# Kernel tuning notes

Hardware: AMD Instinct MI355X
Metric: run time of the kernel (lower is better)

The kernel has to match this reference:

```python
import jax, jax.numpy as jnp
import numpy as np
from jax import lax

N_ENT = 20000; N_REL = 256; H = 512; C = 64; K = 3; L = 2; T = 8; E = 30000; B = 4096


def _seg_mean(vals, ids, num_segments):
    s = jax.ops.segment_sum(vals, ids, num_segments=num_segments)
    c = jax.ops.segment_sum(jnp.ones(ids.shape, vals.dtype), ids, num_segments=num_segments)
    return s / jnp.maximum(c, 1.0)[:, None]


def _normalize(x, eps=1e-8):
    return x / (jnp.linalg.norm(x, axis=-1, keepdims=True) + eps)


def _gru(x, h, Wih, Whh, bih, bhh):
    gi = x @ Wih + bih
    gh = h @ Whh + bhh
    ir, iz, inn = jnp.split(gi, 3, axis=-1)
    hr, hz, hn = jnp.split(gh, 3, axis=-1)
    r = jax.nn.sigmoid(ir + hr)
    z = jax.nn.sigmoid(iz + hz)
    n = jnp.tanh(inn + r * hn)
    return (1.0 - z) * n + z * h


def _backbone(x, convW, convB, fcW, fcB):
    # x: (B, Cin, H) -> (B, H); ConvTrans backbone: 1D 'same' conv over hidden dim,
    # relu, flatten, linear projection back to H, relu (BN identity at init, dropout=eval)
    h = lax.conv_general_dilated(x, convW, (1,), 'SAME', dimension_numbers=('NCH', 'OIH', 'NCH'))
    h = jax.nn.relu(h + convB[None, :, None])
    h = h.reshape(h.shape[0], -1)
    return jax.nn.relu(h @ fcW + fcB)


def _forward(ent_embeds, rel_embeds, W_msg, W_self, gru_Wih, gru_Whh, gru_bih, gru_bhh,
             gate_W, gate_b,
             e_conv1, e_cb1, e_fc1, e_fb1, e_conv2, e_cb2, e_fc2, e_fb2,
             r_conv1, r_cb1, r_fc1, r_fb1, r_conv2, r_cb2, r_fc2, r_fb2,
             src, dst, erel, subj, rel, obj):
    def step(carry, xs):
        ent, relh = carry
        s, d, r = xs
        # relation evolution: aggregate incident-entity embeds per relation, GRU with static rel embeds
        agg = _seg_mean(ent[s], r, N_REL)                                   # (R, H)
        relh = _gru(jnp.concatenate([agg, rel_embeds], -1), relh, gru_Wih, gru_Whh, gru_bih, gru_bhh)
        # entity evolution: L layers of RGCN-style message passing over the snapshot
        h = ent
        for l in range(L):
            msg = (h[s] + relh[r]) @ W_msg[l]                               # (E, H)
            h = jax.nn.relu(_seg_mean(msg, d, N_ENT) + h @ W_self[l])
        h = _normalize(h)
        u = jax.nn.sigmoid(h @ gate_W + gate_b)                             # time gate
        ent = u * h + (1.0 - u) * ent
        return (ent, relh), None

    (ent, relh), _ = lax.scan(step, (_normalize(ent_embeds), rel_embeds), (src, dst, erel))

    se = ent[subj]
    re_ = relh[rel]
    oe = ent[obj]
    # RefineConvTransE (object prediction)
    o1 = _backbone(jnp.stack([se, re_], 1), e_conv1, e_cb1, e_fc1, e_fb1)
    o2 = _backbone(jnp.stack([o1, se, re_], 1), e_conv2, e_cb2, e_fc2, e_fb2)
    # RefineConvTransR (relation prediction)
    q1 = _backbone(jnp.stack([se, oe], 1), r_conv1, r_cb1, r_fc1, r_fb1)
    q2 = _backbone(jnp.stack([q1, se, oe], 1), r_conv2, r_cb2, r_fc2, r_fb2)
    return (o1 @ ent.T, q1 @ relh.T, o2 @ ent.T, q2 @ relh.T)


def setup_inputs() -> dict:
    key = jax.random.key(0)
    ks = jax.random.split(key, 32)
    f = lambda i, shape, s=0.02: jax.random.normal(ks[i], shape, jnp.float32) * s
    return dict(
        ent_embeds=f(0, (N_ENT, H), 0.05),
        rel_embeds=f(1, (N_REL, H), 0.05),
        W_msg=f(2, (L, H, H)),
        W_self=f(3, (L, H, H)),
        gru_Wih=f(4, (2 * H, 3 * H)),
        gru_Whh=f(5, (H, 3 * H)),
        gru_bih=jnp.zeros((3 * H,), jnp.float32),
        gru_bhh=jnp.zeros((3 * H,), jnp.float32),
        gate_W=f(6, (H, H)),
        gate_b=jnp.zeros((H,), jnp.float32),
        e_conv1=f(7, (C, 2, K)), e_cb1=jnp.zeros((C,), jnp.float32),
        e_fc1=f(8, (C * H, H)), e_fb1=jnp.zeros((H,), jnp.float32),
        e_conv2=f(9, (C, 3, K)), e_cb2=jnp.zeros((C,), jnp.float32),
        e_fc2=f(10, (C * H, H)), e_fb2=jnp.zeros((H,), jnp.float32),
        r_conv1=f(11, (C, 2, K)), r_cb1=jnp.zeros((C,), jnp.float32),
        r_fc1=f(12, (C * H, H)), r_fb1=jnp.zeros((H,), jnp.float32),
        r_conv2=f(13, (C, 3, K)), r_cb2=jnp.zeros((C,), jnp.float32),
        r_fc2=f(14, (C * H, H)), r_fb2=jnp.zeros((H,), jnp.float32),
        src=jax.random.randint(ks[15], (T, E), 0, N_ENT),
        dst=jax.random.randint(ks[16], (T, E), 0, N_ENT),
        erel=jax.random.randint(ks[17], (T, E), 0, N_REL),
        subj=jax.random.randint(ks[18], (B,), 0, N_ENT),
        rel=jax.random.randint(ks[19], (B,), 0, N_REL),
        obj=jax.random.randint(ks[20], (B,), 0, N_ENT),
    )


def reference(ent_embeds, rel_embeds, W_msg, W_self, gru_Wih, gru_Whh, gru_bih, gru_bhh,
              gate_W, gate_b,
              e_conv1, e_cb1, e_fc1, e_fb1, e_conv2, e_cb2, e_fc2, e_fb2,
              r_conv1, r_cb1, r_fc1, r_fb1, r_conv2, r_cb2, r_fc2, r_fb2,
              src, dst, erel, subj, rel, obj):
    # returns (obj_logit_ori, rel_logit_ori, obj_logit, rel_logit)
    return _forward(ent_embeds, rel_embeds, W_msg, W_self, gru_Wih, gru_Whh, gru_bih, gru_bhh,
                    gate_W, gate_b,
                    e_conv1, e_cb1, e_fc1, e_fb1, e_conv2, e_cb2, e_fc2, e_fb2,
                    r_conv1, r_cb1, r_fc1, r_fb1, r_conv2, r_cb2, r_fc2, r_fb2,
                    src, dst, erel, subj, rel, obj)
```

## Files before the change

### kernel.cpp

```cpp
#include <hip/hip_runtime.h>
#include <math.h>


#define N_ENT 20000
#define N_REL 256
#define HD    512
#define NE    30000
#define NB    4096
#define NT    8

typedef __attribute__((ext_vector_type(8))) short          bf16x8;
typedef __attribute__((ext_vector_type(4))) float          f32x4;
typedef __attribute__((ext_vector_type(8))) unsigned short u16x8;
typedef __attribute__((ext_vector_type(4))) unsigned short u16x4;

static __device__ __forceinline__ float sigmoidf_(float x) {
  return 1.0f / (1.0f + expf(-x));
}
static __device__ __forceinline__ unsigned short f2bf(float f) {
  unsigned u = __float_as_uint(f);
  return (unsigned short)((u + 0x7FFFu + ((u >> 16) & 1u)) >> 16);
}

__global__ void rownorm_kernel(const float* __restrict__ in, float* __restrict__ out,
                               unsigned short* __restrict__ outb, int rows) {
  int wid = (blockIdx.x * blockDim.x + threadIdx.x) >> 6;
  int lane = threadIdx.x & 63;
  if (wid >= rows) return;
  const float4* ip = (const float4*)(in + (size_t)wid * HD);
  float4 v0 = ip[lane];
  float4 v1 = ip[lane + 64];
  float s = v0.x * v0.x + v0.y * v0.y + v0.z * v0.z + v0.w * v0.w
          + v1.x * v1.x + v1.y * v1.y + v1.z * v1.z + v1.w * v1.w;
  #pragma unroll
  for (int m = 1; m < 64; m <<= 1) s += __shfl_xor(s, m);
  float inv = 1.0f / (sqrtf(s) + 1e-8f);
  float4* op = (float4*)(out + (size_t)wid * HD);
  v0.x *= inv; v0.y *= inv; v0.z *= inv; v0.w *= inv;
  v1.x *= inv; v1.y *= inv; v1.z *= inv; v1.w *= inv;
  op[lane] = v0; op[lane + 64] = v1;
  unsigned short* ob = outb + (size_t)wid * HD;
  u16x4 p0 = {f2bf(v0.x), f2bf(v0.y), f2bf(v0.z), f2bf(v0.w)};
  u16x4 p1 = {f2bf(v1.x), f2bf(v1.y), f2bf(v1.z), f2bf(v1.w)};
  *(u16x4*)&ob[lane * 4] = p0;
  *(u16x4*)&ob[(lane + 64) * 4] = p1;
}

__global__ void zero_hist_all(int* __restrict__ h) {
  int i = blockIdx.x * 256 + threadIdx.x;
  if (i < NT * (N_ENT + N_REL)) h[i] = 0;
}

__global__ void hist_all(const int* __restrict__ dst, const int* __restrict__ rel,
                         int* __restrict__ histD8, int* __restrict__ histR8) {
  int e = blockIdx.x * 256 + threadIdx.x;
  int t = blockIdx.y;
  if (e >= NE) return;
  atomicAdd(&histD8[t * N_ENT + dst[t * NE + e]], 1);
  atomicAdd(&histR8[t * N_REL + rel[t * NE + e]], 1);
}

__global__ void scan_part_all(const int* __restrict__ histD8, int* __restrict__ partD8) {
  int t = blockIdx.x, tid = threadIdx.x;
  const int* hd = histD8 + t * N_ENT;
  int base = tid * 80;
  int s = 0;
  for (int i = 0; i < 80; ++i) {
    int idx = base + i;
    if (idx < N_ENT) s += hd[idx];
  }
  partD8[t * 257 + tid] = s;
}

__global__ void scan_serial_all(int* __restrict__ partD8, const int* __restrict__ histR8,
                                int* __restrict__ startR8, int* __restrict__ posR8) {
  int t = blockIdx.x;
  int* pd = partD8 + t * 257;
  int run = 0;
  for (int i = 0; i < 256; ++i) { int v = pd[i]; pd[i] = run; run += v; }
  pd[256] = run;
  const int* hr = histR8 + t * N_REL;
  int* sr = startR8 + t * 257;
  int* pr = posR8 + t * N_REL;
  run = 0;
  for (int i = 0; i < 256; ++i) { int v = hr[i]; sr[i] = run; pr[i] = run; run += v; }
  sr[256] = run;
}

__global__ void scan_local_all(const int* __restrict__ histD8, const int* __restrict__ partD8,
                               int* __restrict__ startD8, int* __restrict__ posD8) {
  int t = blockIdx.x, tid = threadIdx.x;
  const int* hd = histD8 + t * N_ENT;
  int* sd = startD8 + t * (N_ENT + 1);
  int* pd = posD8 + t * N_ENT;
  int run = partD8[t * 257 + tid];
  int base = tid * 80;
  for (int i = 0; i < 80; ++i) {
    int idx = base + i;
    if (idx < N_ENT) {
      sd[idx] = run;
      pd[idx] = run;
      run += hd[idx];
    }
  }
  if (tid == 0) sd[N_ENT] = partD8[t * 257 + 256];
}

__global__ void scatter_all(const int* __restrict__ dst, const int* __restrict__ rel,
                            int* __restrict__ posD8, int* __restrict__ posR8,
                            int* __restrict__ edgeD8, int* __restrict__ edgeR8) {
  int e = blockIdx.x * 256 + threadIdx.x;
  int t = blockIdx.y;
  if (e >= NE) return;
  int p = atomicAdd(&posD8[t * N_ENT + dst[t * NE + e]], 1);
  edgeD8[t * NE + p] = e;
  int p2 = atomicAdd(&posR8[t * N_REL + rel[t * NE + e]], 1);
  edgeR8[t * NE + p2] = e;
}

__global__ __launch_bounds__(256)
void agg_rel_csr(const float* __restrict__ ent, const int* __restrict__ src,
                 const int* __restrict__ edgeR, const int* __restrict__ startR,
                 float* __restrict__ aggR, float* __restrict__ cntR) {
  int r = blockIdx.x * 4 + (threadIdx.x >> 6);
  if (r >= N_REL) return;
  int lane = threadIdx.x & 63;
  int s0 = startR[r], s1 = startR[r + 1];
  float4 a = make_float4(0.f, 0.f, 0.f, 0.f);
  float4 b = make_float4(0.f, 0.f, 0.f, 0.f);
  for (int i = s0; i < s1; ++i) {
    int e = edgeR[i];
    int s = src[e];
    const float4* p = (const float4*)(ent + (size_t)s * HD);
    float4 x = p[lane];
    float4 y = p[lane + 64];
    a.x += x.x; a.y += x.y; a.z += x.z; a.w += x.w;
    b.x += y.x; b.y += y.y; b.z += y.z; b.w += y.w;
  }
  float4* op = (float4*)(aggR + (size_t)r * HD);
  op[lane] = a;
  op[lane + 64] = b;
  if (lane == 0) cntR[r] = (float)(s1 - s0);
}

__global__ __launch_bounds__(256)
void agg_ent_csr(const float* __restrict__ h, const float* __restrict__ relh,
                 const int* __restrict__ src, const int* __restrict__ erel,
                 const int* __restrict__ edgeD, const int* __restrict__ startD,
                 float* __restrict__ aggE, float* __restrict__ cntE) {
  int d = blockIdx.x * 4 + (threadIdx.x >> 6);
  if (d >= N_ENT) return;
  int lane = threadIdx.x & 63;
  int s0 = startD[d], s1 = startD[d + 1];
  float4 a = make_float4(0.f, 0.f, 0.f, 0.f);
  float4 b = make_float4(0.f, 0.f, 0.f, 0.f);
  for (int i = s0; i < s1; ++i) {
    int e = edgeD[i];
    int s = src[e], r = erel[e];
    const float4* hp = (const float4*)(h + (size_t)s * HD);
    const float4* rp = (const float4*)(relh + (size_t)r * HD);
    float4 x = hp[lane];
    float4 y = hp[lane + 64];
    float4 u = rp[lane];
    float4 v = rp[lane + 64];
    a.x += x.x + u.x; a.y += x.y + u.y; a.z += x.z + u.z; a.w += x.w + u.w;
    b.x += y.x + v.x; b.y += y.y + v.y; b.z += y.z + v.z; b.w += y.w + v.w;
  }
  float4* op = (float4*)(aggE + (size_t)d * HD);
  op[lane] = a;
  op[lane + 64] = b;
  if (lane == 0) cntE[d] = (float)(s1 - s0);
}

__global__ void gru_kernel(const float* __restrict__ gi, const float* __restrict__ gh,
                           const float* __restrict__ bih, const float* __restrict__ bhh,
                           float* __restrict__ relh, unsigned short* __restrict__ relhb) {
  int i = blockIdx.x * blockDim.x + threadIdx.x;
  if (i >= N_REL * HD) return;
  int row = i >> 9, col = i & 511;
  const float* gir = gi + (size_t)row * 1536;
  const float* ghr = gh + (size_t)row * 1536;
  float ir = gir[col] + bih[col];
  float iz = gir[col + 512] + bih[col + 512];
  float inn = gir[col + 1024] + bih[col + 1024];
  float hr = ghr[col] + bhh[col];
  float hz = ghr[col + 512] + bhh[col + 512];
  float hn = ghr[col + 1024] + bhh[col + 1024];
  float r = sigmoidf_(ir + hr);
  float z = sigmoidf_(iz + hz);
  float n = tanhf(inn + r * hn);
  float v = (1.0f - z) * n + z * relh[i];
  relh[i] = v;
  relhb[i] = f2bf(v);
}

__global__ void gather_kernel(const float* __restrict__ table, const int* __restrict__ idx,
                              float* __restrict__ out, int rows) {
  int i = blockIdx.x * blockDim.x + threadIdx.x;
  if (i >= rows * (HD / 4)) return;
  int row = i >> 7, q = i & 127;
  ((float4*)out)[i] = ((const float4*)(table + (size_t)idx[row] * HD))[q];
}

__global__ void f2b_kernel(const float* __restrict__ in, unsigned short* __restrict__ out, int n) {
  int i = blockIdx.x * blockDim.x + threadIdx.x;
  if (i * 8 >= n) return;
  float4 a = *(const float4*)&in[i * 8];
  float4 b = *(const float4*)&in[i * 8 + 4];
  u16x8 pk = {f2bf(a.x), f2bf(a.y), f2bf(a.z), f2bf(a.w),
              f2bf(b.x), f2bf(b.y), f2bf(b.z), f2bf(b.w)};
  *(u16x8*)&out[i * 8] = pk;
}

__global__ void pack_nn_kernel(const float* __restrict__ B, unsigned short* __restrict__ out,
                               int K, int N) {
  int id = blockIdx.x * 256 + threadIdx.x;
  if (id >= (K >> 3) * N) return;
  int s = id / (N * 4);
  int rem = id - s * (N * 4);
  int n = rem >> 2, g = rem & 3;
  const float* src = B + (size_t)(s * 32 + g * 8) * N + n;
  u16x8 pk;
  #pragma unroll
  for (int j = 0; j < 8; ++j) pk[j] = f2bf(src[(size_t)j * N]);
  *(u16x8*)&out[((size_t)s * N + n) * 32 + ((g ^ ((n >> 2) & 3)) << 3)] = pk;
}

template <int ACT, int MIRROR>
static __device__ __forceinline__
void gemm_core(const float* __restrict__ A0, int K0, const float* __restrict__ cntA,
               const unsigned short* __restrict__ A1, int K1,
               const unsigned short* __restrict__ Bp,
               const float* __restrict__ bias, const float* __restrict__ D,
               float* __restrict__ C, unsigned short* __restrict__ Cb,
               int M, int N, int m0, int n0,
               unsigned short (*As)[4096], unsigned short (*Bs)[4096]) {
  const int tid = threadIdx.x;
  const int lane = tid & 63;
  const int wv = tid >> 6;
  const int wm = wv >> 1, wn = wv & 1;
  const int lr = lane & 15, lg = lane >> 4;
  const int arow = tid >> 1;
  const int ahalf = tid & 1;
  const int NIT = (K0 + K1) >> 5;

  float s0 = 1.0f;
  if (K0 > 0 && (m0 + arow) < M) s0 = 1.0f / fmaxf(cntA[m0 + arow], 1.0f);

  f32x4 acc[4][4];
  #pragma unroll
  for (int i = 0; i < 4; ++i)
    #pragma unroll
    for (int j = 0; j < 4; ++j) acc[i][j] = (f32x4){0.f, 0.f, 0.f, 0.f};

  auto gload = [&](int it, u16x8* ar, u16x8* br) {
    int mrow = m0 + arow;
    int kk = it * 32 + ahalf * 16;
    if (mrow < M) {
      if (kk < K0) {
        const float* p = A0 + (size_t)mrow * K0 + kk;
        #pragma unroll
        for (int q = 0; q < 2; ++q) {
          float4 x = *(const float4*)(p + q * 8);
          float4 y = *(const float4*)(p + q * 8 + 4);
          ar[q] = (u16x8){f2bf(x.x * s0), f2bf(x.y * s0), f2bf(x.z * s0), f2bf(x.w * s0),
                          f2bf(y.x * s0), f2bf(y.y * s0), f2bf(y.z * s0), f2bf(y.w * s0)};
        }
      } else {
        const unsigned short* p = A1 + (size_t)mrow * K1 + (kk - K0);
        #pragma unroll
        for (int q = 0; q < 2; ++q) ar[q] = *(const u16x8*)&p[q * 8];
      }
    } else {
      #pragma unroll
      for (int q = 0; q < 2; ++q) ar[q] = (u16x8){0, 0, 0, 0, 0, 0, 0, 0};
    }
    const unsigned short* b0 = Bp + ((size_t)it * N + n0) * 32;
    br[0] = *(const u16x8*)&b0[tid * 8];
    br[1] = *(const u16x8*)&b0[2048 + tid * 8];
  };
  auto swrite = [&](int nb, const u16x8* ar, const u16x8* br) {
    #pragma unroll
    for (int q = 0; q < 2; ++q) {
      int chunk = ahalf * 2 + q;
      *(u16x8*)&As[nb][arow * 32 + ((chunk ^ ((arow >> 1) & 3)) << 3)] = ar[q];
    }
    *(u16x8*)&Bs[nb][tid * 8] = br[0];
    *(u16x8*)&Bs[nb][2048 + tid * 8] = br[1];
  };
  auto mfma_phase = [&](int nb) {
    bf16x8 a[4], b[4];
    #pragma unroll
    for (int i = 0; i < 4; ++i) {
      int r = wm * 64 + i * 16 + lr;
      a[i] = *(const bf16x8*)&As[nb][r * 32 + ((lg ^ ((r >> 1) & 3)) << 3)];
      int nl = wn * 64 + i * 16 + lr;
      b[i] = *(const bf16x8*)&Bs[nb][nl * 32 + ((lg ^ ((nl >> 2) & 3)) << 3)];
    }
    #pragma unroll
    for (int i = 0; i < 4; ++i)
      #pragma unroll
      for (int j = 0; j < 4; ++j)
        acc[i][j] = __builtin_amdgcn_mfma_f32_16x16x32_bf16(a[i], b[j], acc[i][j], 0, 0, 0);
  };

  u16x8 ar0[2], br0[2], ar1[2], br1[2];
  gload(0, ar0, br0);
  swrite(0, ar0, br0);
  gload(1, ar1, br1);
  __syncthreads();

  int cur = 0;
  for (int itp = 0; itp < NIT; itp += 2) {
    if (itp + 2 < NIT) gload(itp + 2, ar0, br0);
    mfma_phase(cur);
    swrite(cur ^ 1, ar1, br1);
    __syncthreads();
    cur ^= 1;
    if (itp + 3 < NIT) gload(itp + 3, ar1, br1);
    mfma_phase(cur);
    if (itp + 2 < NIT) swrite(cur ^ 1, ar0, br0);
    __syncthreads();
    cur ^= 1;
  }

  #pragma unroll
  for (int i = 0; i < 4; ++i) {
    int m = m0 + wm * 64 + i * 16 + lg * 4;
    #pragma unroll
    for (int j = 0; j < 4; ++j) {
      int n = n0 + wn * 64 + j * 16 + lr;
      #pragma unroll
      for (int q = 0; q < 4; ++q) {
        int mr = m + q;
        if (mr >= M) continue;
        size_t o = (size_t)mr * N + n;
        float v = acc[i][j][q];
        if (ACT == 0) {
          C[o] = v;
        } else if (ACT == 1) {
          float rr = fmaxf(v, 0.0f);
          C[o] = rr;
          if (MIRROR) Cb[o] = f2bf(rr);
        } else {
          float u_ = sigmoidf_(v + bias[n]);
          float rr = u_ * D[o] + (1.0f - u_) * C[o];
          C[o] = rr;
          if (MIRROR) Cb[o] = f2bf(rr);
        }
      }
    }
  }
}

template <int ACT, int MIRROR>
__global__ __launch_bounds__(256, 3)
void gemm_nn2(const float* __restrict__ A0, int K0, const float* __restrict__ cntA,
              const unsigned short* __restrict__ A1, int K1,
              const unsigned short* __restrict__ Bp,
              const float* __restrict__ bias, const float* __restrict__ D,
              float* __restrict__ C, unsigned short* __restrict__ Cb, int M, int N) {
  __shared__ unsigned short As[2][4096];
  __shared__ unsigned short Bs[2][4096];
  gemm_core<ACT, MIRROR>(A0, K0, cntA, A1, K1, Bp, bias, D, C, Cb, M, N,
                         blockIdx.x * 128, blockIdx.y * 128, As, Bs);
}

__global__ __launch_bounds__(256, 3)
void gru_gemms(const float* __restrict__ aggR, const float* __restrict__ cntR,
               const unsigned short* __restrict__ rel_bf,
               const unsigned short* __restrict__ relh_bf,
               const unsigned short* __restrict__ wp_ih,
               const unsigned short* __restrict__ wp_hh,
               float* __restrict__ gi, float* __restrict__ gh) {
  __shared__ unsigned short As[2][4096];
  __shared__ unsigned short Bs[2][4096];
  if (blockIdx.z == 0)
    gemm_core<0, 0>(aggR, 512, cntR, rel_bf, 512, wp_ih, nullptr, nullptr,
                    gi, nullptr, N_REL, 1536, blockIdx.x * 128, blockIdx.y * 128, As, Bs);
  else
    gemm_core<0, 0>(nullptr, 0, nullptr, relh_bf, 512, wp_hh, nullptr, nullptr,
                    gh, nullptr, N_REL, 1536, blockIdx.x * 128, blockIdx.y * 128, As, Bs);
}

__global__ __launch_bounds__(256)
void pack_fw_kernel(const float* __restrict__ f0, const float* __restrict__ f1,
                    const float* __restrict__ f2, const float* __restrict__ f3,
                    unsigned short* __restrict__ o0, unsigned short* __restrict__ o1,
                    unsigned short* __restrict__ o2, unsigned short* __restrict__ o3) {
  __shared__ float L[32][512];
  const float* fw; unsigned short* op;
  switch (blockIdx.y) {
    case 0: fw = f0; op = o0; break;
    case 1: fw = f1; op = o1; break;
    case 2: fw = f2; op = o2; break;
    default: fw = f3; op = o3; break;
  }
  int s = blockIdx.x, tid = threadIdx.x;
  #pragma unroll
  for (int i = 0; i < 16; ++i) {
    int idx = tid + 256 * i;
    int r = idx >> 7, cq = (idx & 127) << 2;
    *(float4*)&L[r][cq] = *(const float4*)&fw[(size_t)(s * 32 + r) * 512 + cq];
  }
  __syncthreads();
  #pragma unroll
  for (int ii = 0; ii < 8; ++ii) {
    int slot = tid + 256 * ii;
    int n = slot >> 2, g = slot & 3;
    u16x8 pk;
    #pragma unroll
    for (int j = 0; j < 8; ++j) pk[j] = f2bf(L[g * 8 + j][n]);
    size_t off = (size_t)s * 16384 + n * 32 + ((g ^ ((n >> 2) & 3)) << 3);
    *(u16x8*)&op[off] = pk;
  }
}

template <int CIN>
__global__ __launch_bounds__(256)
void convgen_kernel(const float* __restrict__ X0e, const float* __restrict__ X1e,
                    const float* __restrict__ X2e,
                    const float* __restrict__ cwE, const float* __restrict__ cbE,
                    const float* __restrict__ X0r, const float* __restrict__ X1r,
                    const float* __restrict__ X2r,
                    const float* __restrict__ cwR, const float* __restrict__ cbR,
                    unsigned short* __restrict__ Ae, unsigned short* __restrict__ Ar) {
  __shared__ float wsm[64 * CIN * 3];
  __shared__ float bsm[64];
  const int path = blockIdx.y;
  const float* X[CIN]; const float* cw; const float* cb; unsigned short* A;
  if (path == 0) {
    X[0] = X0e; X[1] = X1e; if constexpr (CIN == 3) X[2] = X2e;
    cw = cwE; cb = cbE; A = Ae;
  } else {
    X[0] = X0r; X[1] = X1r; if constexpr (CIN == 3) X[2] = X2r;
    cw = cwR; cb = cbR; A = Ar;
  }
  const int tid = threadIdx.x;
  for (int i = tid; i < 64 * CIN * 3; i += 256) wsm[i] = cw[i];
  if (tid < 64) bsm[tid] = cb[tid];
  __syncthreads();

  const int o = tid & 63;
  const int b = blockIdx.x * 4 + (tid >> 6);
  const int h = o * 8;

  float xm[CIN][8], xl[CIN], xr[CIN];
  #pragma unroll
  for (int ci = 0; ci < CIN; ++ci) {
    const float* row = X[ci] + (size_t)b * HD + h;
    float4 a4 = *(const float4*)row;
    float4 b4 = *(const float4*)(row + 4);
    xm[ci][0] = a4.x; xm[ci][1] = a4.y; xm[ci][2] = a4.z; xm[ci][3] = a4.w;
    xm[ci][4] = b4.x; xm[ci][5] = b4.y; xm[ci][6] = b4.z; xm[ci][7] = b4.w;
    xl[ci] = (h > 0) ? row[-1] : 0.f;
    xr[ci] = (h + 8 < HD) ? row[8] : 0.f;
  }
  unsigned short* dst = A + (size_t)b * 32768 + h;
  for (int c = 0; c < 64; ++c) {
    float v[8];
    float cbv = bsm[c];
    #pragma unroll
    for (int e = 0; e < 8; ++e) v[e] = cbv;
    #pragma unroll
    for (int ci = 0; ci < CIN; ++ci) {
      float w0 = wsm[(c * CIN + ci) * 3 + 0];
      float w1 = wsm[(c * CIN + ci) * 3 + 1];
      float w2 = wsm[(c * CIN + ci) * 3 + 2];
      #pragma unroll
      for (int e = 0; e < 8; ++e) {
        float lft = e ? xm[ci][e - 1] : xl[ci];
        float rgt = (e < 7) ? xm[ci][e + 1] : xr[ci];
        v[e] = fmaf(lft, w0, fmaf(xm[ci][e], w1, fmaf(rgt, w2, v[e])));
      }
    }
    u16x8 pk;
    #pragma unroll
    for (int e = 0; e < 8; ++e) pk[e] = f2bf(fmaxf(v[e], 0.f));
    *(u16x8*)&dst[c * 512] = pk;
  }
}

__global__ __launch_bounds__(256, 2)
void gemm_fc(const unsigned short* __restrict__ Abuf,
             const unsigned short* __restrict__ fwpE,
             const unsigned short* __restrict__ fwpR,
             float* __restrict__ partBase) {
  __shared__ unsigned short As[2][128 * 64];
  __shared__ unsigned short Bs[2][2 * 128 * 32];
  const int tid = threadIdx.x;
  const int lane = tid & 63;
  const int wv = tid >> 6;
  const int wm = wv >> 1, wn = wv & 1;
  const int lr = lane & 15, lg = lane >> 4;
  const int m0 = blockIdx.x * 128;
  const int n0 = blockIdx.y * 128;
  const int path = blockIdx.z >> 2;
  const int ks = blockIdx.z & 3;

  const unsigned short* A = Abuf + (size_t)path * ((size_t)NB * 32768);
  const unsigned short* fwp = (path == 0) ? fwpE : fwpR;
  float* part = partBase + (size_t)(path * 4 + ks) * ((size_t)NB * HD);

  const int arow = tid >> 1;
  const int achunk = (tid & 1) * 4;
  const unsigned short* aRow = A + (size_t)(m0 + arow) * 32768 + ks * 8192 + achunk * 8;
  const unsigned short* bBase = fwp + (size_t)(ks * 256) * 16384 + (size_t)n0 * 32;

  f32x4 acc[4][4];
  #pragma unroll
  for (int i = 0; i < 4; ++i)
    #pragma unroll
    for (int j = 0; j < 4; ++j) acc[i][j] = (f32x4){0.f, 0.f, 0.f, 0.f};

  auto gload = [&](int it, u16x8* ar, u16x8* br) {
    const unsigned short* ap = aRow + it * 64;
    #pragma unroll
    for (int q = 0; q < 4; ++q) ar[q] = *(const u16x8*)&ap[q * 8];
    const unsigned short* bp = bBase + (size_t)it * 2 * 16384;
    br[0] = *(const u16x8*)&bp[tid * 8];
    br[1] = *(const u16x8*)&bp[2048 + tid * 8];
    br[2] = *(const u16x8*)&bp[16384 + tid * 8];
    br[3] = *(const u16x8*)&bp[16384 + 2048 + tid * 8];
  };
  auto swrite = [&](int nb, const u16x8* ar, const u16x8* br) {
    #pragma unroll
    for (int q = 0; q < 4; ++q) {
      int chunk = achunk + q;
      *(u16x8*)&As[nb][arow * 64 + ((chunk ^ (arow & 7)) << 3)] = ar[q];
    }
    *(u16x8*)&Bs[nb][tid * 8] = br[0];
    *(u16x8*)&Bs[nb][2048 + tid * 8] = br[1];
    *(u16x8*)&Bs[nb][4096 + tid * 8] = br[2];
    *(u16x8*)&Bs[nb][4096 + 2048 + tid * 8] = br[3];
  };
  auto mfma_phase = [&](int nb) {
    bf16x8 af[2][4], bfr[2][4];
    #pragma unroll
    for (int u = 0; u < 2; ++u)
      #pragma unroll
      for (int i = 0; i < 4; ++i) {
        int r = wm * 64 + i * 16 + lr;
        af[u][i] = *(const bf16x8*)&As[nb][r * 64 + (((u * 4 + lg) ^ (r & 7)) << 3)];
        int nl = wn * 64 + i * 16 + lr;
        bfr[u][i] = *(const bf16x8*)&Bs[nb][u * 4096 + nl * 32 + ((lg ^ ((nl >> 2) & 3)) << 3)];
      }
    #pragma unroll
    for (int u = 0; u < 2; ++u)
      #pragma unroll
      for (int i = 0; i < 4; ++i)
        #pragma unroll
        for (int j = 0; j < 4; ++j)
          acc[i][j] = __builtin_amdgcn_mfma_f32_16x16x32_bf16(af[u][i], bfr[u][j], acc[i][j], 0, 0, 0);
  };

  u16x8 ar0[4], br0[4], ar1[4], br1[4];
  gload(0, ar0, br0);
  swrite(0, ar0, br0);
  gload(1, ar1, br1);
  __syncthreads();

  int cur = 0;
  for (int itp = 0; itp < 128; itp += 2) {
    if (itp + 2 < 128) gload(itp + 2, ar0, br0);
    mfma_phase(cur);
    swrite(cur ^ 1, ar1, br1);
    __syncthreads();
    cur ^= 1;
    if (itp + 3 < 128) gload(itp + 3, ar1, br1);
    mfma_phase(cur);
    if (itp + 2 < 128) swrite(cur ^ 1, ar0, br0);
    __syncthreads();
    cur ^= 1;
  }

  #pragma unroll
  for (int i = 0; i < 4; ++i) {
    int m = m0 + wm * 64 + i * 16 + lg * 4;
    #pragma unroll
    for (int j = 0; j < 4; ++j) {
      int n = n0 + wn * 64 + j * 16 + lr;
      #pragma unroll
      for (int q = 0; q < 4; ++q)
        part[(size_t)(m + q) * HD + n] = acc[i][j][q];
    }
  }
}

__global__ void reduce4_kernel(const float* __restrict__ pE, const float* __restrict__ pR,
                               const float* __restrict__ bE, const float* __restrict__ bR,
                               float* __restrict__ oE, float* __restrict__ oR,
                               unsigned short* __restrict__ obE, unsigned short* __restrict__ obR) {
  int p = blockIdx.y;
  const float* part = p ? pR : pE;
  const float* bias = p ? bR : bE;
  float* o = p ? oR : oE;
  unsigned short* ob = p ? obR : obE;
  int i = blockIdx.x * 256 + threadIdx.x;
  int col = (i << 2) & 511;
  float4 s = *(const float4*)&part[(size_t)i * 4];
  #pragma unroll
  for (int ks = 1; ks < 4; ++ks) {
    float4 t = *(const float4*)&part[(size_t)ks * (NB * HD) + i * 4];
    s.x += t.x; s.y += t.y; s.z += t.z; s.w += t.w;
  }
  float4 b4 = *(const float4*)&bias[col];
  s.x = fmaxf(s.x + b4.x, 0.f); s.y = fmaxf(s.y + b4.y, 0.f);
  s.z = fmaxf(s.z + b4.z, 0.f); s.w = fmaxf(s.w + b4.w, 0.f);
  *(float4*)&o[(size_t)i * 4] = s;
  u16x4 pk = {f2bf(s.x), f2bf(s.y), f2bf(s.z), f2bf(s.w)};
  *(u16x4*)&ob[(size_t)i * 4] = pk;
}

__global__ __launch_bounds__(256, 2)
void gemm_nt_bf16(const unsigned short* __restrict__ A, const unsigned short* __restrict__ B,
                  float* __restrict__ C, int M, int N, int K) {
  __shared__ unsigned short As[2][8192];
  __shared__ unsigned short Bs[2][8192];
  const int tid = threadIdx.x;
  const int lane = tid & 63;
  const int wv = tid >> 6;
  const int wm = wv >> 1, wn = wv & 1;
  const int m0 = blockIdx.x * 128, n0 = blockIdx.y * 128;
  const int lr = lane & 15, lg = lane >> 4;
  const int row = tid >> 1, half = tid & 1;
  const int nrow = n0 + row;
  const int NIT = K >> 6;

  f32x4 acc[4][4];
  #pragma unroll
  for (int i = 0; i < 4; ++i)
    #pragma unroll
    for (int j = 0; j < 4; ++j) acc[i][j] = (f32x4){0.f, 0.f, 0.f, 0.f};

  auto gload = [&](int it, u16x8* ar, u16x8* br) {
    const unsigned short* asrc = A + (size_t)(m0 + row) * K + it * 64 + half * 32;
    #pragma unroll
    for (int q = 0; q < 4; ++q) ar[q] = *(const u16x8*)&asrc[q * 8];
    const unsigned short* bsrc = B + (size_t)nrow * K + it * 64 + half * 32;
    u16x8 z = {0, 0, 0, 0, 0, 0, 0, 0};
    #pragma unroll
    for (int q = 0; q < 4; ++q) br[q] = (nrow < N) ? *(const u16x8*)&bsrc[q * 8] : z;
  };
  auto swrite = [&](int nb, const u16x8* ar, const u16x8* br) {
    #pragma unroll
    for (int q = 0; q < 4; ++q) {
      int chunk = half * 4 + q;
      *(u16x8*)&As[nb][row * 64 + ((chunk ^ (row & 7)) << 3)] = ar[q];
      *(u16x8*)&Bs[nb][row * 64 + ((chunk ^ (row & 7)) << 3)] = br[q];
    }
  };
  auto mfma_phase = [&](int nb) {
    #pragma unroll
    for (int u = 0; u < 2; ++u) {
      bf16x8 a[4], b[4];
      #pragma unroll
      for (int i = 0; i < 4; ++i) {
        int r = wm * 64 + i * 16 + lr;
        a[i] = *(const bf16x8*)&As[nb][r * 64 + (((u * 4 + lg) ^ (r & 7)) << 3)];
        int n = wn * 64 + i * 16 + lr;
        b[i] = *(const bf16x8*)&Bs[nb][n * 64 + (((u * 4 + lg) ^ (n & 7)) << 3)];
      }
      #pragma unroll
      for (int i = 0; i < 4; ++i)
        #pragma unroll
        for (int j = 0; j < 4; ++j)
          acc[i][j] = __builtin_amdgcn_mfma_f32_16x16x32_bf16(a[i], b[j], acc[i][j], 0, 0, 0);
    }
  };

  u16x8 ar0[4], br0[4], ar1[4], br1[4];
  gload(0, ar0, br0);
  swrite(0, ar0, br0);
  gload(1, ar1, br1);
  __syncthreads();

  int cur = 0;
  for (int itp = 0; itp < NIT; itp += 2) {
    if (itp + 2 < NIT) gload(itp + 2, ar0, br0);
    mfma_phase(cur);
    swrite(cur ^ 1, ar1, br1);
    __syncthreads();
    cur ^= 1;
    if (itp + 3 < NIT) gload(itp + 3, ar1, br1);
    mfma_phase(cur);
    if (itp + 2 < NIT) swrite(cur ^ 1, ar0, br0);
    __syncthreads();
    cur ^= 1;
  }

  #pragma unroll
  for (int i = 0; i < 4; ++i) {
    int m = m0 + wm * 64 + i * 16 + lg * 4;
    #pragma unroll
    for (int j = 0; j < 4; ++j) {
      int n = n0 + wn * 64 + j * 16 + lr;
      if (n < N) {
        #pragma unroll
        for (int q = 0; q < 4; ++q)
          C[(size_t)(m + q) * N + n] = acc[i][j][q];
      }
    }
  }
}

extern "C" void kernel_launch(void* const* d_in, const int* in_sizes, int n_in,
                              void* d_out, int out_size, void* d_ws, size_t ws_size,
                              hipStream_t stream) {
  const float* ent_embeds = (const float*)d_in[0];
  const float* rel_embeds = (const float*)d_in[1];
  const float* W_msg  = (const float*)d_in[2];
  const float* W_self = (const float*)d_in[3];
  const float* gru_Wih = (const float*)d_in[4];
  const float* gru_Whh = (const float*)d_in[5];
  const float* gru_bih = (const float*)d_in[6];
  const float* gru_bhh = (const float*)d_in[7];
  const float* gate_W = (const float*)d_in[8];
  const float* gate_b = (const float*)d_in[9];
  const float* e_conv1 = (const float*)d_in[10]; const float* e_cb1 = (const float*)d_in[11];
  const float* e_fc1   = (const float*)d_in[12]; const float* e_fb1 = (const float*)d_in[13];
  const float* e_conv2 = (const float*)d_in[14]; const float* e_cb2 = (const float*)d_in[15];
  const float* e_fc2   = (const float*)d_in[16]; const float* e_fb2 = (const float*)d_in[17];
  const float* r_conv1 = (const float*)d_in[18]; const float* r_cb1 = (const float*)d_in[19];
  const float* r_fc1   = (const float*)d_in[20]; const float* r_fb1 = (const float*)d_in[21];
  const float* r_conv2 = (const float*)d_in[22]; const float* r_cb2 = (const float*)d_in[23];
  const float* r_fc2   = (const float*)d_in[24]; const float* r_fb2 = (const float*)d_in[25];
  const int* src  = (const int*)d_in[26];
  const int* dst  = (const int*)d_in[27];
  const int* erel = (const int*)d_in[28];
  const int* subj = (const int*)d_in[29];
  const int* rel  = (const int*)d_in[30];
  const int* obj  = (const int*)d_in[31];
  float* out = (float*)d_out;

  float* w = (float*)d_ws;
  float* ent   = w; w += (size_t)N_ENT * HD;
  float* relh  = w; w += (size_t)N_REL * HD;
  float* aggR  = w; w += (size_t)N_REL * HD;
  float* cntR  = w; w += N_REL;
  float* gi    = w; w += (size_t)N_REL * 1536;
  float* gh    = w; w += (size_t)N_REL * 1536;
  float* aggE  = w; w += (size_t)N_ENT * HD;
  float* cntE  = w; w += N_ENT;
  float* tmp   = w; w += (size_t)N_ENT * HD;
  float* h0b   = w; w += (size_t)N_ENT * HD;
  float* h1b   = w; w += (size_t)N_ENT * HD;
  float* se    = w; w += (size_t)NB * HD;
  float* re_   = w; w += (size_t)NB * HD;
  float* oe    = w; w += (size_t)NB * HD;
  float* o1    = w; w += (size_t)NB * HD;
  float* q1    = w; w += (size_t)NB * HD;
  float* o2    = w; w += (size_t)NB * HD;
  float* q2    = w; w += (size_t)NB * HD;
  unsigned short* ent_bf  = (unsigned short*)w; w += (size_t)N_ENT * HD / 2;
  unsigned short* relh_bf = (unsigned short*)w; w += (size_t)N_REL * HD / 2;
  unsigned short* rel_bf  = (unsigned short*)w; w += (size_t)N_REL * HD / 2;
  unsigned short* h0b_bf  = (unsigned short*)w; w += (size_t)N_ENT * HD / 2;
  unsigned short* h1b_bf  = (unsigned short*)w; w += (size_t)N_ENT * HD / 2;
  unsigned short* o1b = (unsigned short*)w; w += (size_t)NB * HD / 2;
  unsigned short* q1b = (unsigned short*)w; w += (size_t)NB * HD / 2;
  unsigned short* o2b = (unsigned short*)w; w += (size_t)NB * HD / 2;
  unsigned short* q2b = (unsigned short*)w; w += (size_t)NB * HD / 2;
  unsigned short* wp_ih = (unsigned short*)w;
  unsigned short* wp_hh = wp_ih + (size_t)1024 * 1536;
  unsigned short* wp_l0 = wp_hh + (size_t)512 * 1536;
  unsigned short* wp_l1 = wp_l0 + (size_t)1024 * 512;
  unsigned short* wp_g  = wp_l1 + (size_t)1024 * 512;
  w += ((size_t)1024 * 1536 + 512 * 1536 + 2 * 1024 * 512 + 512 * 512) / 2;
  int* histD8  = (int*)w;
  int* histR8  = histD8 + (size_t)NT * N_ENT;
  int* partD8  = histR8 + (size_t)NT * N_REL;
  int* startD8 = partD8 + (size_t)NT * 257;
  int* posD8   = startD8 + (size_t)NT * (N_ENT + 1);
  int* startR8 = posD8 + (size_t)NT * N_ENT;
  int* posR8   = startR8 + (size_t)NT * 257;
  int* edgeD8  = posR8 + (size_t)NT * N_REL;
  int* edgeR8  = edgeD8 + (size_t)NT * NE;
  unsigned short* fwp0 = (unsigned short*)aggE;
  unsigned short* fwp1 = fwp0 + (size_t)16777216;
  unsigned short* fwp2 = fwp1 + (size_t)16777216;
  unsigned short* fwp3 = fwp2 + (size_t)16777216;
  (void)tmp;
  unsigned short* Abuf = (unsigned short*)out;
  float* pE = out + (size_t)2 * NB * 32768 / 2;
  float* pR = pE + (size_t)4 * NB * HD;

  const dim3 g_gru(2, 12, 2);
  const dim3 g_ent(157, 4);

  {
    int t;
    t = (1024 * 1536) / 8; pack_nn_kernel<<<(t + 255) / 256, 256, 0, stream>>>(gru_Wih, wp_ih, 1024, 1536);
    t = (512 * 1536) / 8;  pack_nn_kernel<<<(t + 255) / 256, 256, 0, stream>>>(gru_Whh, wp_hh, 512, 1536);
    t = (512 * 512) / 8;
    pack_nn_kernel<<<(t + 255) / 256, 256, 0, stream>>>(W_msg, wp_l0, 512, 512);
    pack_nn_kernel<<<(t + 255) / 256, 256, 0, stream>>>(W_self, wp_l0 + (size_t)512 * 512, 512, 512);
    pack_nn_kernel<<<(t + 255) / 256, 256, 0, stream>>>(W_msg + (size_t)512 * 512, wp_l1, 512, 512);
    pack_nn_kernel<<<(t + 255) / 256, 256, 0, stream>>>(W_self + (size_t)512 * 512, wp_l1 + (size_t)512 * 512, 512, 512);
    pack_nn_kernel<<<(t + 255) / 256, 256, 0, stream>>>(gate_W, wp_g, 512, 512);
  }

  zero_hist_all<<<(NT * (N_ENT + N_REL) + 255) / 256, 256, 0, stream>>>(histD8);
  hist_all<<<dim3((NE + 255) / 256, NT), 256, 0, stream>>>(dst, erel, histD8, histR8);
  scan_part_all<<<NT, 256, 0, stream>>>(histD8, partD8);
  scan_serial_all<<<NT, 1, 0, stream>>>(partD8, histR8, startR8, posR8);
  scan_local_all<<<NT, 256, 0, stream>>>(histD8, partD8, startD8, posD8);
  scatter_all<<<dim3((NE + 255) / 256, NT), 256, 0, stream>>>(dst, erel, posD8, posR8,
                                                              edgeD8, edgeR8);

  rownorm_kernel<<<N_ENT / 4, 256, 0, stream>>>(ent_embeds, ent, ent_bf, N_ENT);
  hipMemcpyAsync(relh, rel_embeds, (size_t)N_REL * HD * 4, hipMemcpyDeviceToDevice, stream);
  f2b_kernel<<<(N_REL * HD / 8) / 256, 256, 0, stream>>>(rel_embeds, rel_bf, N_REL * HD);
  f2b_kernel<<<(N_REL * HD / 8) / 256, 256, 0, stream>>>(rel_embeds, relh_bf, N_REL * HD);

  for (int t = 0; t < NT; ++t) {
    const int* st = src + t * NE;
    const int* rt = erel + t * NE;
    const int* edgeD = edgeD8 + (size_t)t * NE;
    const int* edgeR = edgeR8 + (size_t)t * NE;
    const int* startD = startD8 + (size_t)t * (N_ENT + 1);
    const int* startR = startR8 + (size_t)t * 257;

    agg_rel_csr<<<N_REL / 4, 256, 0, stream>>>(ent, st, edgeR, startR, aggR, cntR);
    gru_gemms<<<g_gru, 256, 0, stream>>>(aggR, cntR, rel_bf, relh_bf, wp_ih, wp_hh, gi, gh);
    gru_kernel<<<(N_REL * HD) / 256, 256, 0, stream>>>(gi, gh, gru_bih, gru_bhh, relh, relh_bf);

    agg_ent_csr<<<N_ENT / 4, 256, 0, stream>>>(ent, relh, st, rt, edgeD, startD, aggE, cntE);
    gemm_nn2<1, 1><<<g_ent, 256, 0, stream>>>(aggE, 512, cntE, ent_bf, 512, wp_l0,
                                              nullptr, nullptr, h0b, h0b_bf, N_ENT, 512);
    agg_ent_csr<<<N_ENT / 4, 256, 0, stream>>>(h0b, relh, st, rt, edgeD, startD, aggE, cntE);
    gemm_nn2<1, 0><<<g_ent, 256, 0, stream>>>(aggE, 512, cntE, h0b_bf, 512, wp_l1,
                                              nullptr, nullptr, h1b, nullptr, N_ENT, 512);
    rownorm_kernel<<<N_ENT / 4, 256, 0, stream>>>(h1b, h1b, h1b_bf, N_ENT);
    gemm_nn2<3, 1><<<g_ent, 256, 0, stream>>>(nullptr, 0, nullptr, h1b_bf, 512, wp_g,
                                              gate_b, h1b, ent, ent_bf, N_ENT, 512);
  }

  pack_fw_kernel<<<dim3(1024, 4), 256, 0, stream>>>(e_fc1, r_fc1, e_fc2, r_fc2,
                                                    fwp0, fwp1, fwp2, fwp3);
  gather_kernel<<<(NB * HD / 4) / 256, 256, 0, stream>>>(ent, subj, se, NB);
  gather_kernel<<<(NB * HD / 4) / 256, 256, 0, stream>>>(relh, rel, re_, NB);
  gather_kernel<<<(NB * HD / 4) / 256, 256, 0, stream>>>(ent, obj, oe, NB);

  unsigned short* A_E = Abuf;
  unsigned short* A_R = Abuf + (size_t)NB * 32768;

  convgen_kernel<2><<<dim3(NB / 4, 2), 256, 0, stream>>>(
      se, re_, nullptr, e_conv1, e_cb1,
      se, oe, nullptr, r_conv1, r_cb1, A_E, A_R);
  gemm_fc<<<dim3(32, 4, 8), 256, 0, stream>>>(Abuf, fwp0, fwp1, pE);
  reduce4_kernel<<<dim3(NB * HD / 4 / 256, 2), 256, 0, stream>>>(
      pE, pR, e_fb1, r_fb1, o1, q1, o1b, q1b);

  convgen_kernel<3><<<dim3(NB / 4, 2), 256, 0, stream>>>(
      o1, se, re_, e_conv2, e_cb2,
      q1, se, oe, r_conv2, r_cb2, A_E, A_R);
  gemm_fc<<<dim3(32, 4, 8), 256, 0, stream>>>(Abuf, fwp2, fwp3, pE);
  reduce4_kernel<<<dim3(NB * HD / 4 / 256, 2), 256, 0, stream>>>(
      pE, pR, e_fb2, r_fb2, o2, q2, o2b, q2b);

  size_t off0 = 0;
  size_t off1 = (size_t)NB * N_ENT;
  size_t off2 = off1 + (size_t)NB * N_REL;
  size_t off3 = off2 + (size_t)NB * N_ENT;
  gemm_nt_bf16<<<dim3(32, 157), 256, 0, stream>>>(o1b, ent_bf, out + off0, NB, N_ENT, HD);
  gemm_nt_bf16<<<dim3(32, 2), 256, 0, stream>>>(q1b, relh_bf, out + off1, NB, N_REL, HD);
  gemm_nt_bf16<<<dim3(32, 157), 256, 0, stream>>>(o2b, ent_bf, out + off2, NB, N_ENT, HD);
  gemm_nt_bf16<<<dim3(32, 2), 256, 0, stream>>>(q2b, relh_bf, out + off3, NB, N_REL, HD);
}
```

Measured before the change: 4.134 ms.

## Fuse row normalization into GEMM epilogues and batch final score GEMMs

The layer-1 GEMM epilogue now writes per-row partial sums of squares into a small buffer. The gate GEMM reads these to compute the L2 norm scale inline. It applies the scale both to its fp32 A operand, converted on load, and to the D term in its epilogue. This removes the separate rownorm kernel and the h1b bf16 mirror each timestep. Separately, the paired final scoring GEMMs are merged into single launches using blockIdx.z, which cuts launch count and improves occupancy for the small relation GEMMs. The gate GEMM now loads fp32 A and converts it, adding some load bandwidth.

```diff
diff --git a/kernel.cpp b/kernel.cpp
--- a/kernel.cpp
+++ b/kernel.cpp
@@ -226,13 +226,14 @@
   *(u16x8*)&out[((size_t)s * N + n) * 32 + ((g ^ ((n >> 2) & 3)) << 3)] = pk;
 }
 
-template <int ACT, int MIRROR>
+template <int ACT, int MIRROR, int SCALEMODE, int WNRM>
 static __device__ __forceinline__
-void gemm_core(const float* __restrict__ A0, int K0, const float* __restrict__ cntA,
+void gemm_core(const float* __restrict__ A0, int K0, const float* __restrict__ scl,
                const unsigned short* __restrict__ A1, int K1,
                const unsigned short* __restrict__ Bp,
                const float* __restrict__ bias, const float* __restrict__ D,
                float* __restrict__ C, unsigned short* __restrict__ Cb,
+               float* __restrict__ pnrm, int nslot,
                int M, int N, int m0, int n0,
                unsigned short (*As)[4096], unsigned short (*Bs)[4096]) {
   const int tid = threadIdx.x;
@@ -245,7 +246,14 @@
   const int NIT = (K0 + K1) >> 5;
 
   float s0 = 1.0f;
-  if (K0 > 0 && (m0 + arow) < M) s0 = 1.0f / fmaxf(cntA[m0 + arow], 1.0f);
+  if (SCALEMODE == 1 && K0 > 0 && (m0 + arow) < M) {
+    s0 = 1.0f / fmaxf(scl[m0 + arow], 1.0f);
+  } else if (SCALEMODE == 2 && K0 > 0 && (m0 + arow) < M) {
+    float tsum = 0.f;
+    #pragma unroll
+    for (int k2 = 0; k2 < 8; ++k2) tsum += scl[(size_t)(m0 + arow) * 8 + k2];
+    s0 = 1.0f / (sqrtf(tsum) + 1e-8f);
+  }
 
   f32x4 acc[4][4];
   #pragma unroll
@@ -324,9 +332,30 @@
     cur ^= 1;
   }
 
+  float psq[4][4];
+  if (WNRM) {
+    #pragma unroll
+    for (int i = 0; i < 4; ++i)
+      #pragma unroll
+      for (int q = 0; q < 4; ++q) psq[i][q] = 0.f;
+  }
+
   #pragma unroll
   for (int i = 0; i < 4; ++i) {
     int m = m0 + wm * 64 + i * 16 + lg * 4;
+    float sn[4];
+    if (ACT == 3 && SCALEMODE == 2) {
+      #pragma unroll
+      for (int q = 0; q < 4; ++q) {
+        int mr = m + q;
+        if (mr < M) {
+          float tsum = 0.f;
+          #pragma unroll
+          for (int k2 = 0; k2 < 8; ++k2) tsum += scl[(size_t)mr * 8 + k2];
+          sn[q] = 1.0f / (sqrtf(tsum) + 1e-8f);
+        } else sn[q] = 1.0f;
+      }
+    }
     #pragma unroll
     for (int j = 0; j < 4; ++j) {
       int n = n0 + wn * 64 + j * 16 + lr;
@@ -342,28 +371,52 @@
           float rr = fmaxf(v, 0.0f);
           C[o] = rr;
           if (MIRROR) Cb[o] = f2bf(rr);
+          if (WNRM) psq[i][q] += rr * rr;
         } else {
           float u_ = sigmoidf_(v + bias[n]);
-          float rr = u_ * D[o] + (1.0f - u_) * C[o];
+          float dv = (SCALEMODE == 2) ? D[o] * sn[q] : D[o];
+          float rr = u_ * dv + (1.0f - u_) * C[o];
           C[o] = rr;
           if (MIRROR) Cb[o] = f2bf(rr);
         }
       }
     }
   }
-}
-
-template <int ACT, int MIRROR>
+
+  if (WNRM) {
+    #pragma unroll
+    for (int mm = 1; mm < 16; mm <<= 1) {
+      #pragma unroll
+      for (int i = 0; i < 4; ++i)
+        #pragma unroll
+        for (int q = 0; q < 4; ++q)
+          psq[i][q] += __shfl_xor(psq[i][q], mm);
+    }
+    if (lr == 0) {
+      #pragma unroll
+      for (int i = 0; i < 4; ++i)
+        #pragma unroll
+        for (int q = 0; q < 4; ++q) {
+          int mr = m0 + wm * 64 + i * 16 + lg * 4 + q;
+          if (mr < M) pnrm[(size_t)mr * 8 + nslot * 2 + wn] = psq[i][q];
+        }
+    }
+  }
+}
+
+template <int ACT, int MIRROR, int SCALEMODE, int WNRM>
 __global__ __launch_bounds__(256, 3)
-void gemm_nn2(const float* __restrict__ A0, int K0, const float* __restrict__ cntA,
+void gemm_nn2(const float* __restrict__ A0, int K0, const float* __restrict__ scl,
               const unsigned short* __restrict__ A1, int K1,
               const unsigned short* __restrict__ Bp,
               const float* __restrict__ bias, const float* __restrict__ D,
-              float* __restrict__ C, unsigned short* __restrict__ Cb, int M, int N) {
+              float* __restrict__ C, unsigned short* __restrict__ Cb,
+              float* __restrict__ pnrm, int M, int N) {
   __shared__ unsigned short As[2][4096];
   __shared__ unsigned short Bs[2][4096];
-  gemm_core<ACT, MIRROR>(A0, K0, cntA, A1, K1, Bp, bias, D, C, Cb, M, N,
-                         blockIdx.x * 128, blockIdx.y * 128, As, Bs);
+  gemm_core<ACT, MIRROR, SCALEMODE, WNRM>(A0, K0, scl, A1, K1, Bp, bias, D, C, Cb,
+                                          pnrm, blockIdx.y, M, N,
+                                          blockIdx.x * 128, blockIdx.y * 128, As, Bs);
 }
 
 __global__ __launch_bounds__(256, 3)
@@ -376,11 +429,13 @@
   __shared__ unsigned short As[2][4096];
   __shared__ unsigned short Bs[2][4096];
   if (blockIdx.z == 0)
-    gemm_core<0, 0>(aggR, 512, cntR, rel_bf, 512, wp_ih, nullptr, nullptr,
-                    gi, nullptr, N_REL, 1536, blockIdx.x * 128, blockIdx.y * 128, As, Bs);
+    gemm_core<0, 0, 1, 0>(aggR, 512, cntR, rel_bf, 512, wp_ih, nullptr, nullptr,
+                          gi, nullptr, nullptr, 0, N_REL, 1536,
+                          blockIdx.x * 128, blockIdx.y * 128, As, Bs);
   else
-    gemm_core<0, 0>(nullptr, 0, nullptr, relh_bf, 512, wp_hh, nullptr, nullptr,
-                    gh, nullptr, N_REL, 1536, blockIdx.x * 128, blockIdx.y * 128, As, Bs);
+    gemm_core<0, 0, 0, 0>(nullptr, 0, nullptr, relh_bf, 512, wp_hh, nullptr, nullptr,
+                          gh, nullptr, nullptr, 0, N_REL, 1536,
+                          blockIdx.x * 128, blockIdx.y * 128, As, Bs);
 }
 
 __global__ __launch_bounds__(256)
@@ -613,10 +668,14 @@
 }
 
 __global__ __launch_bounds__(256, 2)
-void gemm_nt_bf16(const unsigned short* __restrict__ A, const unsigned short* __restrict__ B,
-                  float* __restrict__ C, int M, int N, int K) {
+void gemm_nt_bf16(const unsigned short* __restrict__ Aa, const unsigned short* __restrict__ Ab,
+                  const unsigned short* __restrict__ B,
+                  float* __restrict__ Ca, float* __restrict__ Cb2,
+                  int M, int N, int K) {
   __shared__ unsigned short As[2][8192];
   __shared__ unsigned short Bs[2][8192];
+  const unsigned short* A = (blockIdx.z == 0) ? Aa : Ab;
+  float* C = (blockIdx.z == 0) ? Ca : Cb2;
   const int tid = threadIdx.x;
   const int lane = tid & 63;
   const int wv = tid >> 6;
@@ -756,11 +815,11 @@
   unsigned short* relh_bf = (unsigned short*)w; w += (size_t)N_REL * HD / 2;
   unsigned short* rel_bf  = (unsigned short*)w; w += (size_t)N_REL * HD / 2;
   unsigned short* h0b_bf  = (unsigned short*)w; w += (size_t)N_ENT * HD / 2;
-  unsigned short* h1b_bf  = (unsigned short*)w; w += (size_t)N_ENT * HD / 2;
   unsigned short* o1b = (unsigned short*)w; w += (size_t)NB * HD / 2;
   unsigned short* q1b = (unsigned short*)w; w += (size_t)NB * HD / 2;
   unsigned short* o2b = (unsigned short*)w; w += (size_t)NB * HD / 2;
   unsigned short* q2b = (unsigned short*)w; w += (size_t)NB * HD / 2;
+  float* pnrm = w; w += (size_t)N_ENT * 8;
   unsigned short* wp_ih = (unsigned short*)w;
   unsigned short* wp_hh = wp_ih + (size_t)1024 * 1536;
   unsigned short* wp_l0 = wp_hh + (size_t)512 * 1536;
@@ -826,14 +885,16 @@
     gru_kernel<<<(N_REL * HD) / 256, 256, 0, stream>>>(gi, gh, gru_bih, gru_bhh, relh, relh_bf);
 
     agg_ent_csr<<<N_ENT / 4, 256, 0, stream>>>(ent, relh, st, rt, edgeD, startD, aggE, cntE);
-    gemm_nn2<1, 1><<<g_ent, 256, 0, stream>>>(aggE, 512, cntE, ent_bf, 512, wp_l0,
-                                              nullptr, nullptr, h0b, h0b_bf, N_ENT, 512);
+    gemm_nn2<1, 1, 1, 0><<<g_ent, 256, 0, stream>>>(aggE, 512, cntE, ent_bf, 512, wp_l0,
+                                                    nullptr, nullptr, h0b, h0b_bf,
+                                                    nullptr, N_ENT, 512);
     agg_ent_csr<<<N_ENT / 4, 256, 0, stream>>>(h0b, relh, st, rt, edgeD, startD, aggE, cntE);
-    gemm_nn2<1, 0><<<g_ent, 256, 0, stream>>>(aggE, 512, cntE, h0b_bf, 512, wp_l1,
-                                              nullptr, nullptr, h1b, nullptr, N_ENT, 512);
-    rownorm_kernel<<<N_ENT / 4, 256, 0, stream>>>(h1b, h1b, h1b_bf, N_ENT);
-    gemm_nn2<3, 1><<<g_ent, 256, 0, stream>>>(nullptr, 0, nullptr, h1b_bf, 512, wp_g,
-                                              gate_b, h1b, ent, ent_bf, N_ENT, 512);
+    gemm_nn2<1, 0, 1, 1><<<g_ent, 256, 0, stream>>>(aggE, 512, cntE, h0b_bf, 512, wp_l1,
+                                                    nullptr, nullptr, h1b, nullptr,
+                                                    pnrm, N_ENT, 512);
+    gemm_nn2<3, 1, 2, 0><<<g_ent, 256, 0, stream>>>(h1b, 512, pnrm, nullptr, 0, wp_g,
+                                                    gate_b, h1b, ent, ent_bf,
+                                                    nullptr, N_ENT, 512);
   }
 
   pack_fw_kernel<<<dim3(1024, 4), 256, 0, stream>>>(e_fc1, r_fc1, e_fc2, r_fc2,
@@ -863,8 +924,8 @@
   size_t off1 = (size_t)NB * N_ENT;
   size_t off2 = off1 + (size_t)NB * N_REL;
   size_t off3 = off2 + (size_t)NB * N_ENT;
-  gemm_nt_bf16<<<dim3(32, 157), 256, 0, stream>>>(o1b, ent_bf, out + off0, NB, N_ENT, HD);
-  gemm_nt_bf16<<<dim3(32, 2), 256, 0, stream>>>(q1b, relh_bf, out + off1, NB, N_REL, HD);
-  gemm_nt_bf16<<<dim3(32, 157), 256, 0, stream>>>(o2b, ent_bf, out + off2, NB, N_ENT, HD);
-  gemm_nt_bf16<<<dim3(32, 2), 256, 0, stream>>>(q2b, relh_bf, out + off3, NB, N_REL, HD);
-}
+  gemm_nt_bf16<<<dim3(32, 157, 2), 256, 0, stream>>>(o1b, o2b, ent_bf,
+                                                     out + off0, out + off2, NB, N_ENT, HD);
+  gemm_nt_bf16<<<dim3(32, 2, 2), 256, 0, stream>>>(q1b, q2b, relh_bf,
+                                                   out + off1, out + off3, NB, N_REL, HD);
+}
```

Measured after the change: 4.100 ms. About the same (-0.8%).
